# Optimization experiments

Hardware: AMD Instinct MI355X
Metric: run time of the kernel (lower is better)

Reference implementation:

```python
import math
import jax, jax.numpy as jnp
import numpy as np

N_KINDS = 8
D_MODEL = 256
B_FEAT = 24  # Fourier bands; MLP input dim is 2*B_FEAT
SIGMA = 8.0


def setup_inputs() -> dict:
    key = jax.random.key(0)
    ks = jax.random.split(key, 8)
    N, S = 32, 2048
    values = jax.random.normal(ks[0], (N, S, 1), dtype=jnp.float32)
    kinds = jax.random.randint(ks[1], (N, S), 0, N_KINDS, dtype=jnp.int32)
    # Frozen Fourier projection matrix (torch: randn(in_dim, B) * sigma, requires_grad=False)
    Bmat = jax.random.normal(ks[2], (1, B_FEAT), dtype=jnp.float32) * SIGMA
    # Kind embedding table
    kind_emb = jax.random.normal(ks[3], (N_KINDS, D_MODEL), dtype=jnp.float32) * 0.02
    # Per-kind two-layer MLP params
    W1 = jax.random.normal(ks[4], (N_KINDS, 2 * B_FEAT, D_MODEL), dtype=jnp.float32) / math.sqrt(2 * B_FEAT)
    b1 = jnp.zeros((N_KINDS, D_MODEL), dtype=jnp.float32)
    W2 = jax.random.normal(ks[5], (N_KINDS, D_MODEL, D_MODEL), dtype=jnp.float32) / math.sqrt(D_MODEL)
    b2 = jnp.zeros((N_KINDS, D_MODEL), dtype=jnp.float32)
    return {"values": values, "kinds": kinds, "Bmat": Bmat,
            "kind_emb": kind_emb, "W1": W1, "b1": b1, "W2": W2, "b2": b2}


def reference(values, kinds, Bmat, kind_emb, W1, b1, W2, b2):
    N, S, _ = values.shape
    T = N * S
    d = kind_emb.shape[-1]
    # Fourier features: [T, 2B]
    y = (2.0 * math.pi) * values.reshape(T, 1) @ Bmat  # [T, B]
    ff = jnp.concatenate([jnp.sin(y), jnp.cos(y)], axis=-1)  # [T, 2B]
    kinds_flat = kinds.reshape(T)
    out = jnp.zeros((T, d), dtype=values.dtype)
    # kinds partition the tokens, so masked combine == the torch scatter-assign
    for k in range(kind_emb.shape[0]):
        h = jax.nn.gelu(ff @ W1[k] + b1[k], approximate=False)  # torch GELU is exact erf
        o = h @ W2[k] + b2[k]  # [T, d]
        out = jnp.where((kinds_flat == k)[:, None], o, out)
    return out.reshape(N, S, d) + kind_emb[kinds]
```

## Files before the change

kernel.cpp:

```cpp
#include <hip/hip_runtime.h>
#include <hip/hip_bf16.h>
#include <math.h>


#define NK 8
#define DM 256
#define TMAX 65536
#define NBLK 256
#define W1PK 16384
#define W2PK 65536
#define LDSTRIDE 262

typedef __attribute__((ext_vector_type(8))) short   s16x8;
typedef __attribute__((ext_vector_type(8))) __bf16  bf16x8;
typedef __attribute__((ext_vector_type(4))) float   f32x4;
typedef __attribute__((ext_vector_type(2))) float   f32x2;
typedef __attribute__((ext_vector_type(4))) int     i32x4;

__device__ int   g_counts[NK];
__device__ __align__(16) int g_blkcnt[NBLK][NK];
__device__ int   g_bucket[(size_t)NK * TMAX];
__device__ __align__(16) short g_W1p[(size_t)NK * W1PK];
__device__ __align__(16) short g_W2p[(size_t)NK * W2PK];

static __device__ __forceinline__ short f2bf(float f) {
    __hip_bfloat16 h = __float2bfloat16(f);
    return __builtin_bit_cast(short, h);
}

static __device__ __forceinline__ f32x4 mfma16(s16x8 a, s16x8 b, f32x4 c) {
    return __builtin_amdgcn_mfma_f32_16x16x32_bf16(
        __builtin_bit_cast(bf16x8, a), __builtin_bit_cast(bf16x8, b), c, 0, 0, 0);
}

static __device__ __forceinline__ float gelu_fast(float x) {
    float t1 = x * x;
    float m  = fmaf(0.0713548162726f, t1, 1.59576912161f);
    float z  = m * x;
    float e  = __expf(-z);
    return x * __frcp_rn(1.0f + e);
}

__global__ __launch_bounds__(256) void prep_kernel(const float* __restrict__ W1,
                                                   const float* __restrict__ W2,
                                                   const int* __restrict__ kinds, int T) {
    __shared__ float ld[32 * LDSTRIDE];
    __shared__ int wcnt[4][NK];
    const int tid = threadIdx.x;
    const int bid = blockIdx.x;
    if (bid < 80) {
        const int isW1 = (bid >= 64);
        int kind, kt;
        if (isW1) { kind = (bid - 64) >> 1; kt = (bid - 64) & 1; }
        else      { kind = bid >> 3;        kt = bid & 7; }
        #pragma unroll
        for (int i = 0; i < 8; ++i) {
            int f = tid + i * 256;
            int row = f >> 6, col = (f & 63) * 4;
            int kk = kt * 32 + row;
            f32x4 v = (f32x4){0.f, 0.f, 0.f, 0.f};
            if (isW1) {
                if (kk < 48) v = *(const f32x4*)(W1 + ((size_t)kind * 48 + kk) * DM + col);
            } else {
                v = *(const f32x4*)(W2 + ((size_t)kind * DM + kk) * DM + col);
            }
            float* dst = &ld[row * LDSTRIDE + col];
            *(f32x2*)dst       = (f32x2){v[0], v[1]};
            *(f32x2*)(dst + 2) = (f32x2){v[2], v[3]};
        }
        __syncthreads();
        short* outp = isW1 ? (g_W1p + (size_t)kind * W1PK) : (g_W2p + (size_t)kind * W2PK);
        #pragma unroll
        for (int i = 0; i < 4; ++i) {
            int g = tid + i * 256;
            int ntile = g >> 6, l = g & 63;
            int kk0 = (l >> 4) * 8, n = ntile * 16 + (l & 15);
            s16x8 v;
            #pragma unroll
            for (int j = 0; j < 8; ++j) v[j] = f2bf(ld[(kk0 + j) * LDSTRIDE + n]);
            *(s16x8*)(outp + ((size_t)(kt * 16 + ntile) * 64 + l) * 8) = v;
        }
    } else {
        const int b = bid - 80;
        const int wave = tid >> 6, lane = tid & 63;
        int t = b * 256 + tid;
        int k = (t < T) ? kinds[t] : -1;
        #pragma unroll
        for (int kk = 0; kk < NK; ++kk) {
            unsigned long long m = __ballot(k == kk);
            if (lane == 0) wcnt[wave][kk] = __popcll(m);
        }
        __syncthreads();
        if (tid < NK) {
            int s = 0;
            #pragma unroll
            for (int w = 0; w < 4; ++w) s += wcnt[w][tid];
            g_blkcnt[b][tid] = s;
        }
    }
}

__global__ __launch_bounds__(256) void scatter_kernel(const int* __restrict__ kinds, int T) {
    __shared__ int cnt_s[NBLK * NK];
    __shared__ int wcnt[4][NK];
    __shared__ int base_s[NK];
    const int tid = threadIdx.x, wave = tid >> 6, lane = tid & 63;
    const int b = blockIdx.x;
    {
        const i32x4* src = (const i32x4*)&g_blkcnt[0][0];
        i32x4* dst = (i32x4*)cnt_s;
        dst[tid]       = src[tid];
        dst[tid + 256] = src[tid + 256];
    }
    int t = b * 256 + tid;
    int k = (t < T) ? kinds[t] : -1;
    int rank = 0;
    #pragma unroll
    for (int kk = 0; kk < NK; ++kk) {
        unsigned long long m = __ballot(k == kk);
        if (lane == 0) wcnt[wave][kk] = __popcll(m);
        if (k == kk) rank = __popcll(m & ((1ull << lane) - 1ull));
    }
    __syncthreads();
    if (tid < NK) {
        int s = 0;
        for (int bb = 0; bb < NBLK; ++bb) {
            if (bb == b) base_s[tid] = s;
            s += cnt_s[bb * NK + tid];
        }
        if (b == 0) g_counts[tid] = s;
        int ws = 0;
        #pragma unroll
        for (int w = 0; w < 4; ++w) { int c = wcnt[w][tid]; wcnt[w][tid] = ws; ws += c; }
    }
    __syncthreads();
    if (k >= 0)
        g_bucket[(size_t)k * T + base_s[k] + wcnt[wave][k] + rank] = t;
}

__global__ __launch_bounds__(256, 4) void fproj_gemm(
    const float* __restrict__ values, const float* __restrict__ Bmat,
    const float* __restrict__ kind_emb, const float* __restrict__ b1,
    const float* __restrict__ b2, float* __restrict__ out, int T)
{
    int cnts[NK];
    #pragma unroll
    for (int i = 0; i < NK; ++i) cnts[i] = g_counts[i];
    const int bid = blockIdx.x;
    int k = -1, m0 = 0, cum = 0, cnt = 0;
    #pragma unroll
    for (int kk = 0; kk < NK; ++kk) {
        int tk = (cnts[kk] + 31) >> 5;
        if (k < 0 && bid < cum + tk) { k = kk; m0 = (bid - cum) * 32; cnt = cnts[kk]; }
        cum += tk;
    }
    if (k < 0) return;
    const int valid = min(32, cnt - m0);
    const int* buck = g_bucket + (size_t)k * T + m0;

    __shared__ short Hpack[8192];
    short* Apack = Hpack;

    const int tid  = threadIdx.x;
    const int wave = tid >> 6;
    const int lane = tid & 63;
    const int quad = lane >> 4;
    const int cl   = lane & 15;

    const s16x8* B1p = (const s16x8*)(g_W1p + (size_t)k * W1PK);
    s16x8 b1f[2][4];
    #pragma unroll
    for (int kt = 0; kt < 2; ++kt)
        #pragma unroll
        for (int nt = 0; nt < 4; ++nt)
            b1f[kt][nt] = B1p[(kt * 16 + wave * 4 + nt) * 64 + lane];

    #pragma unroll
    for (int i = 0; i < 8; ++i) {
        int idx = tid + i * 256;
        int m = idx >> 6, kk = idx & 63;
        float f = 0.0f;
        if (kk < 48) {
            float v = 0.0f;
            if (m < valid) v = values[buck[m]];
            int b = (kk < 24) ? kk : kk - 24;
            float y = 6.283185307179586f * v * Bmat[b];
            f = (kk < 24) ? __sinf(y) : __cosf(y);
        }
        int mt = m >> 4, kt = kk >> 5, q = (kk >> 3) & 3, j = kk & 7;
        int l = (m & 15) | (q << 4);
        Apack[((kt * 2 + mt) << 9) + (l << 3) + j] = f2bf(f);
    }
    __syncthreads();

    f32x4 acc[2][4];
    #pragma unroll
    for (int mt = 0; mt < 2; ++mt)
        #pragma unroll
        for (int nt = 0; nt < 4; ++nt) acc[mt][nt] = (f32x4){0.f, 0.f, 0.f, 0.f};

    const s16x8* Ap = (const s16x8*)Apack;
    #pragma unroll
    for (int kt = 0; kt < 2; ++kt) {
        s16x8 a[2];
        #pragma unroll
        for (int mt = 0; mt < 2; ++mt) a[mt] = Ap[(kt * 2 + mt) * 64 + lane];
        #pragma unroll
        for (int mt = 0; mt < 2; ++mt)
            #pragma unroll
            for (int nt = 0; nt < 4; ++nt) acc[mt][nt] = mfma16(a[mt], b1f[kt][nt], acc[mt][nt]);
    }
    __syncthreads();

    #pragma unroll
    for (int nt = 0; nt < 4; ++nt) {
        int c = wave * 64 + nt * 16 + cl;
        float bias = b1[k * DM + c];
        int kt2 = c >> 5, q2 = (c >> 3) & 3, j2 = c & 7;
        #pragma unroll
        for (int mt = 0; mt < 2; ++mt)
            #pragma unroll
            for (int r4 = 0; r4 < 4; ++r4) {
                int r = mt * 16 + quad * 4 + r4;
                float h = gelu_fast(acc[mt][nt][r4] + bias);
                int l2 = (r & 15) | (q2 << 4);
                Hpack[((kt2 * 2 + mt) << 9) + (l2 << 3) + j2] = f2bf(h);
            }
    }
    __syncthreads();

    float addc[4];
    #pragma unroll
    for (int nt = 0; nt < 4; ++nt) {
        int c = wave * 64 + nt * 16 + cl;
        addc[nt] = b2[k * DM + c] + kind_emb[k * DM + c];
    }

    f32x4 acc2[2][4];
    #pragma unroll
    for (int mt = 0; mt < 2; ++mt)
        #pragma unroll
        for (int nt = 0; nt < 4; ++nt) acc2[mt][nt] = (f32x4){0.f, 0.f, 0.f, 0.f};

    const s16x8* Hp  = (const s16x8*)Hpack;
    const s16x8* B2p = (const s16x8*)(g_W2p + (size_t)k * W2PK);
    s16x8 bcur[4], bnxt[4];
    #pragma unroll
    for (int nt = 0; nt < 4; ++nt) bcur[nt] = B2p[(wave * 4 + nt) * 64 + lane];
    #pragma unroll
    for (int kt = 0; kt < 8; ++kt) {
        if (kt < 7) {
            #pragma unroll
            for (int nt = 0; nt < 4; ++nt)
                bnxt[nt] = B2p[((kt + 1) * 16 + wave * 4 + nt) * 64 + lane];
        }
        s16x8 a[2];
        #pragma unroll
        for (int mt = 0; mt < 2; ++mt) a[mt] = Hp[(kt * 2 + mt) * 64 + lane];
        #pragma unroll
        for (int mt = 0; mt < 2; ++mt)
            #pragma unroll
            for (int nt = 0; nt < 4; ++nt) acc2[mt][nt] = mfma16(a[mt], bcur[nt], acc2[mt][nt]);
        #pragma unroll
        for (int nt = 0; nt < 4; ++nt) bcur[nt] = bnxt[nt];
    }

    #pragma unroll
    for (int mt = 0; mt < 2; ++mt)
        #pragma unroll
        for (int r4 = 0; r4 < 4; ++r4) {
            int r = mt * 16 + quad * 4 + r4;
            if (r < valid) {
                size_t row = (size_t)buck[r] * DM;
                #pragma unroll
                for (int nt = 0; nt < 4; ++nt) {
                    int c = wave * 64 + nt * 16 + cl;
                    __builtin_nontemporal_store(acc2[mt][nt][r4] + addc[nt], out + row + c);
                }
            }
        }
}

extern "C" void kernel_launch(void* const* d_in, const int* in_sizes, int n_in,
                              void* d_out, int out_size, void* d_ws, size_t ws_size,
                              hipStream_t stream) {
    const float* values   = (const float*)d_in[0];
    const int*   kinds    = (const int*)  d_in[1];
    const float* Bmat     = (const float*)d_in[2];
    const float* kind_emb = (const float*)d_in[3];
    const float* W1       = (const float*)d_in[4];
    const float* b1       = (const float*)d_in[5];
    const float* W2       = (const float*)d_in[6];
    const float* b2       = (const float*)d_in[7];
    float* out = (float*)d_out;
    const int T = in_sizes[0];

    prep_kernel<<<dim3(80 + NBLK), dim3(256), 0, stream>>>(W1, W2, kinds, T);
    scatter_kernel<<<dim3(NBLK), dim3(256), 0, stream>>>(kinds, T);
    fproj_gemm<<<dim3(T / 32 + NK), dim3(256), 0, stream>>>(values, Bmat, kind_emb,
                                                            b1, b2, out, T);
}
```

Before: 127.9 us.

## Halve GEMM row tile, build Fourier operands in registers, parallelize bucket prefix

The main kernel's row tile shrinks from 32 to 16 tokens, doubling the number of blocks. Fourier-feature A fragments are now built directly in registers using hardware fract/sin/cos in revolution units, which removes the LDS staging pass and a barrier. The serial 256-step prefix scan in the scatter kernel becomes a two-level chunked scan. A cheaper round-to-bf16 replaces the library conversion, and the explicit W2 register prefetch is dropped. The trade-off is that each W2 fragment is reused across half as many rows, so W2 traffic per token doubles.

```diff
diff --git a/kernel.cpp b/kernel.cpp
--- a/kernel.cpp
+++ b/kernel.cpp
@@ -26,6 +26,11 @@
 static __device__ __forceinline__ short f2bf(float f) {
     __hip_bfloat16 h = __float2bfloat16(f);
     return __builtin_bit_cast(short, h);
+}
+
+static __device__ __forceinline__ short pkbf(float f) {
+    unsigned u = __builtin_bit_cast(unsigned, f);
+    return (short)((u + 0x8000u) >> 16);
 }
 
 static __device__ __forceinline__ f32x4 mfma16(s16x8 a, s16x8 b, f32x4 c) {
@@ -102,6 +107,8 @@
 
 __global__ __launch_bounds__(256) void scatter_kernel(const int* __restrict__ kinds, int T) {
     __shared__ int cnt_s[NBLK * NK];
+    __shared__ int chunksum[32][NK];
+    __shared__ int chunkpref[32][NK];
     __shared__ int wcnt[4][NK];
     __shared__ int base_s[NK];
     const int tid = threadIdx.x, wave = tid >> 6, lane = tid & 63;
@@ -122,13 +129,23 @@
         if (k == kk) rank = __popcll(m & ((1ull << lane) - 1ull));
     }
     __syncthreads();
+    {
+        int kk = tid & 7, ch = tid >> 3;
+        int s = 0;
+        #pragma unroll
+        for (int i = 0; i < 8; ++i) s += cnt_s[(ch * 8 + i) * NK + kk];
+        chunksum[ch][kk] = s;
+    }
+    __syncthreads();
     if (tid < NK) {
         int s = 0;
-        for (int bb = 0; bb < NBLK; ++bb) {
-            if (bb == b) base_s[tid] = s;
-            s += cnt_s[bb * NK + tid];
-        }
+        #pragma unroll
+        for (int ch = 0; ch < 32; ++ch) { chunkpref[ch][tid] = s; s += chunksum[ch][tid]; }
         if (b == 0) g_counts[tid] = s;
+        int ch = b >> 3;
+        int s2 = chunkpref[ch][tid];
+        for (int bb = ch * 8; bb < b; ++bb) s2 += cnt_s[bb * NK + tid];
+        base_s[tid] = s2;
         int ws = 0;
         #pragma unroll
         for (int w = 0; w < 4; ++w) { int c = wcnt[w][tid]; wcnt[w][tid] = ws; ws += c; }
@@ -150,16 +167,15 @@
     int k = -1, m0 = 0, cum = 0, cnt = 0;
     #pragma unroll
     for (int kk = 0; kk < NK; ++kk) {
-        int tk = (cnts[kk] + 31) >> 5;
-        if (k < 0 && bid < cum + tk) { k = kk; m0 = (bid - cum) * 32; cnt = cnts[kk]; }
+        int tk = (cnts[kk] + 15) >> 4;
+        if (k < 0 && bid < cum + tk) { k = kk; m0 = (bid - cum) * 16; cnt = cnts[kk]; }
         cum += tk;
     }
     if (k < 0) return;
-    const int valid = min(32, cnt - m0);
+    const int valid = min(16, cnt - m0);
     const int* buck = g_bucket + (size_t)k * T + m0;
 
-    __shared__ short Hpack[8192];
-    short* Apack = Hpack;
+    __shared__ short Hpack[4096];
 
     const int tid  = threadIdx.x;
     const int wave = tid >> 6;
@@ -167,65 +183,45 @@
     const int quad = lane >> 4;
     const int cl   = lane & 15;
 
+    float v = 0.0f;
+    if (cl < valid) v = values[buck[cl]];
+    s16x8 a0, a1;
+    #pragma unroll
+    for (int j = 0; j < 8; ++j) {
+        int b0 = (quad == 3) ? j : quad * 8 + j;
+        float r0 = __builtin_amdgcn_fractf(v * Bmat[b0]);
+        float s0 = __builtin_amdgcn_sinf(r0);
+        float c0 = __builtin_amdgcn_cosf(r0);
+        a0[j] = pkbf((quad == 3) ? c0 : s0);
+        int b1i = min(8 * (quad + 1) + j, 23);
+        float r1 = __builtin_amdgcn_fractf(v * Bmat[b1i]);
+        float c1 = __builtin_amdgcn_cosf(r1);
+        a1[j] = pkbf((quad < 2) ? c1 : 0.0f);
+    }
+
+    f32x4 acc[4];
+    #pragma unroll
+    for (int nt = 0; nt < 4; ++nt) acc[nt] = (f32x4){0.f, 0.f, 0.f, 0.f};
     const s16x8* B1p = (const s16x8*)(g_W1p + (size_t)k * W1PK);
-    s16x8 b1f[2][4];
-    #pragma unroll
-    for (int kt = 0; kt < 2; ++kt)
-        #pragma unroll
-        for (int nt = 0; nt < 4; ++nt)
-            b1f[kt][nt] = B1p[(kt * 16 + wave * 4 + nt) * 64 + lane];
-
-    #pragma unroll
-    for (int i = 0; i < 8; ++i) {
-        int idx = tid + i * 256;
-        int m = idx >> 6, kk = idx & 63;
-        float f = 0.0f;
-        if (kk < 48) {
-            float v = 0.0f;
-            if (m < valid) v = values[buck[m]];
-            int b = (kk < 24) ? kk : kk - 24;
-            float y = 6.283185307179586f * v * Bmat[b];
-            f = (kk < 24) ? __sinf(y) : __cosf(y);
-        }
-        int mt = m >> 4, kt = kk >> 5, q = (kk >> 3) & 3, j = kk & 7;
-        int l = (m & 15) | (q << 4);
-        Apack[((kt * 2 + mt) << 9) + (l << 3) + j] = f2bf(f);
-    }
-    __syncthreads();
-
-    f32x4 acc[2][4];
-    #pragma unroll
-    for (int mt = 0; mt < 2; ++mt)
-        #pragma unroll
-        for (int nt = 0; nt < 4; ++nt) acc[mt][nt] = (f32x4){0.f, 0.f, 0.f, 0.f};
-
-    const s16x8* Ap = (const s16x8*)Apack;
-    #pragma unroll
-    for (int kt = 0; kt < 2; ++kt) {
-        s16x8 a[2];
-        #pragma unroll
-        for (int mt = 0; mt < 2; ++mt) a[mt] = Ap[(kt * 2 + mt) * 64 + lane];
-        #pragma unroll
-        for (int mt = 0; mt < 2; ++mt)
-            #pragma unroll
-            for (int nt = 0; nt < 4; ++nt) acc[mt][nt] = mfma16(a[mt], b1f[kt][nt], acc[mt][nt]);
-    }
-    __syncthreads();
+    #pragma unroll
+    for (int nt = 0; nt < 4; ++nt)
+        acc[nt] = mfma16(a0, B1p[(wave * 4 + nt) * 64 + lane], acc[nt]);
+    #pragma unroll
+    for (int nt = 0; nt < 4; ++nt)
+        acc[nt] = mfma16(a1, B1p[(16 + wave * 4 + nt) * 64 + lane], acc[nt]);
 
     #pragma unroll
     for (int nt = 0; nt < 4; ++nt) {
         int c = wave * 64 + nt * 16 + cl;
         float bias = b1[k * DM + c];
         int kt2 = c >> 5, q2 = (c >> 3) & 3, j2 = c & 7;
-        #pragma unroll
-        for (int mt = 0; mt < 2; ++mt)
-            #pragma unroll
-            for (int r4 = 0; r4 < 4; ++r4) {
-                int r = mt * 16 + quad * 4 + r4;
-                float h = gelu_fast(acc[mt][nt][r4] + bias);
-                int l2 = (r & 15) | (q2 << 4);
-                Hpack[((kt2 * 2 + mt) << 9) + (l2 << 3) + j2] = f2bf(h);
-            }
+        short* hp = Hpack + kt2 * 512 + (q2 << 4) * 8 + j2;
+        #pragma unroll
+        for (int r = 0; r < 4; ++r) {
+            int m = quad * 4 + r;
+            float h = gelu_fast(acc[nt][r] + bias);
+            hp[m * 8] = pkbf(h);
+        }
     }
     __syncthreads();
 
@@ -236,49 +232,31 @@
         addc[nt] = b2[k * DM + c] + kind_emb[k * DM + c];
     }
 
-    f32x4 acc2[2][4];
-    #pragma unroll
-    for (int mt = 0; mt < 2; ++mt)
-        #pragma unroll
-        for (int nt = 0; nt < 4; ++nt) acc2[mt][nt] = (f32x4){0.f, 0.f, 0.f, 0.f};
-
+    f32x4 acc2[4];
+    #pragma unroll
+    for (int nt = 0; nt < 4; ++nt) acc2[nt] = (f32x4){0.f, 0.f, 0.f, 0.f};
     const s16x8* Hp  = (const s16x8*)Hpack;
     const s16x8* B2p = (const s16x8*)(g_W2p + (size_t)k * W2PK);
-    s16x8 bcur[4], bnxt[4];
-    #pragma unroll
-    for (int nt = 0; nt < 4; ++nt) bcur[nt] = B2p[(wave * 4 + nt) * 64 + lane];
     #pragma unroll
     for (int kt = 0; kt < 8; ++kt) {
-        if (kt < 7) {
+        s16x8 a = Hp[kt * 64 + lane];
+        #pragma unroll
+        for (int nt = 0; nt < 4; ++nt)
+            acc2[nt] = mfma16(a, B2p[(kt * 16 + wave * 4 + nt) * 64 + lane], acc2[nt]);
+    }
+
+    #pragma unroll
+    for (int r = 0; r < 4; ++r) {
+        int row = quad * 4 + r;
+        if (row < valid) {
+            size_t ro = (size_t)buck[row] * DM;
             #pragma unroll
-            for (int nt = 0; nt < 4; ++nt)
-                bnxt[nt] = B2p[((kt + 1) * 16 + wave * 4 + nt) * 64 + lane];
-        }
-        s16x8 a[2];
-        #pragma unroll
-        for (int mt = 0; mt < 2; ++mt) a[mt] = Hp[(kt * 2 + mt) * 64 + lane];
-        #pragma unroll
-        for (int mt = 0; mt < 2; ++mt)
-            #pragma unroll
-            for (int nt = 0; nt < 4; ++nt) acc2[mt][nt] = mfma16(a[mt], bcur[nt], acc2[mt][nt]);
-        #pragma unroll
-        for (int nt = 0; nt < 4; ++nt) bcur[nt] = bnxt[nt];
-    }
-
-    #pragma unroll
-    for (int mt = 0; mt < 2; ++mt)
-        #pragma unroll
-        for (int r4 = 0; r4 < 4; ++r4) {
-            int r = mt * 16 + quad * 4 + r4;
-            if (r < valid) {
-                size_t row = (size_t)buck[r] * DM;
-                #pragma unroll
-                for (int nt = 0; nt < 4; ++nt) {
-                    int c = wave * 64 + nt * 16 + cl;
-                    __builtin_nontemporal_store(acc2[mt][nt][r4] + addc[nt], out + row + c);
-                }
+            for (int nt = 0; nt < 4; ++nt) {
+                int c = wave * 64 + nt * 16 + cl;
+                __builtin_nontemporal_store(acc2[nt][r] + addc[nt], out + ro + c);
             }
         }
+    }
 }
 
 extern "C" void kernel_launch(void* const* d_in, const int* in_sizes, int n_in,
@@ -297,6 +275,6 @@
 
     prep_kernel<<<dim3(80 + NBLK), dim3(256), 0, stream>>>(W1, W2, kinds, T);
     scatter_kernel<<<dim3(NBLK), dim3(256), 0, stream>>>(kinds, T);
-    fproj_gemm<<<dim3(T / 32 + NK), dim3(256), 0, stream>>>(values, Bmat, kind_emb,
+    fproj_gemm<<<dim3(T / 16 + NK), dim3(256), 0, stream>>>(values, Bmat, kind_emb,
                                                             b1, b2, out, T);
 }
```

Result: faster. 122.6 us (-4.1%).
